# Kernel tuning notes

Measured on AMD Instinct MI355X. Metric: run time of the kernel, lower is better.

The kernel has to match this reference:

```python
import jax, jax.numpy as jnp
import numpy as np

HIDDEN, KEY_DIM, VALUE_DIM = 1024, 64, 64
B, T = 4, 4096


def setup_inputs() -> dict:
    key = jax.random.key(0)
    ks = jax.random.split(key, 9)
    s = 0.02
    return {
        "y_all": jax.random.normal(ks[0], (B, T, HIDDEN), dtype=jnp.float32),
        # torch nn.Linear weights: (out_features, in_features)
        "Wq": jax.random.normal(ks[1], (KEY_DIM, HIDDEN), dtype=jnp.float32) * s,
        "bq": jax.random.normal(ks[2], (KEY_DIM,), dtype=jnp.float32) * s,
        "Wk": jax.random.normal(ks[3], (KEY_DIM, HIDDEN), dtype=jnp.float32) * s,
        "bk": jax.random.normal(ks[4], (KEY_DIM,), dtype=jnp.float32) * s,
        "Wv": jax.random.normal(ks[5], (VALUE_DIM, HIDDEN), dtype=jnp.float32) * s,
        "bv": jax.random.normal(ks[6], (VALUE_DIM,), dtype=jnp.float32) * s,
        "Wo": jax.random.normal(ks[7], (HIDDEN, VALUE_DIM), dtype=jnp.float32) * s,
        "bo": jax.random.normal(ks[8], (HIDDEN,), dtype=jnp.float32) * s,
    }


def reference(y_all, Wq, bq, Wk, bk, Wv, bv, Wo, bo):
    # The original per-timestep loop is exactly causal self-attention:
    # query at position i attends over positions 0..i.
    q = jnp.einsum("bth,kh->btk", y_all, Wq) + bq          # (B,T,Dk)
    k = jnp.einsum("bth,kh->btk", y_all, Wk) + bk          # (B,T,Dk)
    v = jnp.einsum("bth,vh->btv", y_all, Wv) + bv          # (B,T,Dv)
    scale = jnp.asarray(KEY_DIM, q.dtype) ** 0.5
    scores = jnp.einsum("bqk,btk->bqt", q / scale, k)      # (B,T,T)
    t = scores.shape[-1]
    causal = jnp.tril(jnp.ones((t, t), dtype=bool))
    scores = jnp.where(causal, scores, jnp.asarray(-jnp.inf, scores.dtype))
    weights = jax.nn.softmax(scores, axis=-1)
    ctx = jnp.einsum("bqt,btv->bqv", weights, v)           # (B,T,Dv)
    out = jnp.einsum("bqv,hv->bqh", ctx, Wo) + bo          # (B,T,H)
    return out
```

## Files before the change

kernel.cpp:

```cpp
#include <hip/hip_runtime.h>


typedef __attribute__((ext_vector_type(4)))  float f32x4;
typedef __attribute__((ext_vector_type(16))) float f32x16;
typedef __attribute__((ext_vector_type(8)))  short s16x8;
typedef __attribute__((ext_vector_type(4)))  short s16x4;

#define DEV static __device__ __forceinline__

static constexpr int TT = 4096;
static constexpr int HH = 1024;
static constexpr int DD = 64;
static constexpr float MNEG = -3.0e38f;

DEV unsigned short f2bf(float f) {
  union { float f; unsigned int u; } v; v.f = f;
  unsigned int r = v.u + 0x7FFFu + ((v.u >> 16) & 1u);
  return (unsigned short)(r >> 16);
}

DEV unsigned int pk2(float lo, float hi) {
  return (unsigned int)f2bf(lo) | ((unsigned int)f2bf(hi) << 16);
}

DEV s16x8 mk8(unsigned int w0, unsigned int w1, unsigned int w2, unsigned int w3) {
  union { unsigned int u[4]; s16x8 v; } c;
  c.u[0] = w0; c.u[1] = w1; c.u[2] = w2; c.u[3] = w3; return c.v;
}

DEV int swzA(int row) { return ((row & 7) << 4); }
DEV int swzK(int row) { return ((row & 7) << 4) ^ ((row & 8) << 3); }

__global__ void prep_kernel(const float* __restrict__ Wq, const float* __restrict__ Wk,
                            const float* __restrict__ Wv, const float* __restrict__ Wo,
                            unsigned short* __restrict__ Wall,
                            unsigned short* __restrict__ Wo_b)
{
  int i = blockIdx.x * blockDim.x + threadIdx.x;
  int stride = gridDim.x * blockDim.x;
  const int n1 = 64 * HH;
  for (int idx = i; idx < 3 * n1; idx += stride) {
    float v = idx < n1 ? Wq[idx] : (idx < 2 * n1 ? Wk[idx - n1] : Wv[idx - 2 * n1]);
    Wall[idx] = f2bf(v);
  }
  for (int idx = i; idx < HH * DD; idx += stride) {
    int hcol = idx >> 6, d = idx & 63;
    size_t off = (size_t)(hcol >> 4) * 1024 + (d >> 5) * 512 + (hcol & 15) * 32
               + ((d >> 3) & 3) * 8 + (d & 7);
    Wo_b[off] = f2bf(Wo[idx]);
  }
}

__global__ __launch_bounds__(256) void qkv_kernel(
    const float* __restrict__ y, const unsigned short* __restrict__ Wall,
    const float* __restrict__ bq, const float* __restrict__ bk,
    const float* __restrict__ bv,
    unsigned short* __restrict__ q_ws, unsigned short* __restrict__ k_ws,
    unsigned short* __restrict__ vT_ws)
{
  __shared__ unsigned short ylds[2][64 * 64];
  __shared__ unsigned short wlds[2][192 * 64];
  const int t = threadIdx.x;
  const int w = t >> 6, lane = t & 63, g = lane >> 4, c = lane & 15;
  const int row0 = blockIdx.x * 64;
  const int yrow = t >> 2, ycol0 = (t & 3) * 16;

  f32x4 acc[12];
#pragma unroll
  for (int i = 0; i < 12; ++i)
#pragma unroll
    for (int e = 0; e < 4; ++e) acc[i][e] = 0.0f;

  f32x4 yr[4];
  s16x8 wr[6];

  auto load_tiles = [&](int kb) {
    const float* src = y + (size_t)(row0 + yrow) * HH + kb * 64 + ycol0;
    yr[0] = *(const f32x4*)(src);
    yr[1] = *(const f32x4*)(src + 4);
    yr[2] = *(const f32x4*)(src + 8);
    yr[3] = *(const f32x4*)(src + 12);
#pragma unroll
    for (int ii = 0; ii < 6; ++ii) {
      int ch = t + ii * 256;
      int rw = ch >> 3, c0 = (ch & 7) * 8;
      wr[ii] = *(const s16x8*)(Wall + (size_t)rw * HH + kb * 64 + c0);
    }
  };
  auto write_tiles = [&](int buf) {
    s16x8 h0, h1;
#pragma unroll
    for (int e = 0; e < 4; ++e) {
      h0[e]     = (short)f2bf(yr[0][e]);
      h0[e + 4] = (short)f2bf(yr[1][e]);
      h1[e]     = (short)f2bf(yr[2][e]);
      h1[e + 4] = (short)f2bf(yr[3][e]);
    }
    int byte0 = yrow * 128 + ycol0 * 2;
    *(s16x8*)((char*)ylds[buf] + (byte0 ^ swzA(yrow)))        = h0;
    *(s16x8*)((char*)ylds[buf] + ((byte0 + 16) ^ swzA(yrow))) = h1;
#pragma unroll
    for (int ii = 0; ii < 6; ++ii) {
      int ch = t + ii * 256;
      int rw = ch >> 3, c0 = (ch & 7) * 8;
      int byte = rw * 128 + c0 * 2;
      *(s16x8*)((char*)wlds[buf] + (byte ^ swzA(rw))) = wr[ii];
    }
  };

  load_tiles(0);
  write_tiles(0);
  __syncthreads();
  for (int kb = 0; kb < 16; ++kb) {
    int buf = kb & 1;
    if (kb < 15) load_tiles(kb + 1);
#pragma unroll
    for (int kk = 0; kk < 2; ++kk) {
      int r = 16 * w + c;
      s16x8 a = *(const s16x8*)((char*)ylds[buf] +
                  ((r * 128 + (kk * 32 + 8 * g) * 2) ^ swzA(r)));
#pragma unroll
      for (int nt = 0; nt < 12; ++nt) {
        int rb = 16 * nt + c;
        s16x8 b = *(const s16x8*)((char*)wlds[buf] +
                    ((rb * 128 + (kk * 32 + 8 * g) * 2) ^ swzA(rb)));
        acc[nt] = __builtin_amdgcn_mfma_f32_16x16x32_bf16(a, b, acc[nt], 0, 0, 0);
      }
    }
    __syncthreads();
    if (kb < 15) { write_tiles((kb + 1) & 1); __syncthreads(); }
  }

  const float qsc = 1.4426950408889634f / 8.0f;
  const int bb = row0 >> 12;
  const int tb = row0 & 4095;
#pragma unroll
  for (int nt = 0; nt < 12; ++nt) {
    int sec = nt >> 2;
    int dcol = (nt & 3) * 16 + c;
    float bias = sec == 0 ? bq[dcol] : (sec == 1 ? bk[dcol] : bv[dcol]);
    if (sec == 2) {
      s16x4 pv;
#pragma unroll
      for (int i = 0; i < 4; ++i) pv[i] = (short)f2bf(acc[nt][i] + bias);
      int t0 = tb + 16 * w + 4 * g;
      size_t off = (size_t)bb * (DD * TT) + (size_t)(t0 >> 6) * 4096
                 + (dcol >> 5) * 2048 + w * 512 + (dcol & 31) * 16 + (t0 & 15);
      *(s16x4*)(vT_ws + off) = pv;
    } else {
      unsigned short* dst = sec == 0 ? q_ws : k_ws;
      int kk = nt & 3;
#pragma unroll
      for (int i = 0; i < 4; ++i) {
        int t_in = tb + 16 * w + 4 * g + i;
        float val = acc[nt][i] + bias;
        if (sec == 0) val *= qsc;
        size_t off = (size_t)bb * (TT * DD) + (size_t)(t_in >> 5) * 2048
                   + kk * 512 + (t_in & 31) * 16 + c;
        dst[off] = f2bf(val);
      }
    }
  }
}

__global__ __launch_bounds__(256, 2) void attn_kernel(
    const unsigned short* __restrict__ q_ws, const unsigned short* __restrict__ k_ws,
    const unsigned short* __restrict__ vT_ws, const unsigned short* __restrict__ Wo_b,
    const float* __restrict__ bo, float* __restrict__ out)
{
  __shared__ float obuf[3 * 2048];
  __shared__ float mstat[3 * 128];
  __shared__ unsigned short clds[32 * 64];
  const int t = threadIdx.x, wv = t >> 6, lane = t & 63;
  const int qcol = lane & 31, h = lane >> 5;
  const int b = blockIdx.x & 3;
  const int jslot = blockIdx.x >> 2;
  const int j32 = (jslot < 64) ? (2 * jslot) : (127 - 2 * (jslot - 64));
  const int q0 = j32 * 32;
  const int L = j32 >> 1;
  const size_t base  = (size_t)b * TT * DD;
  const size_t vbase = (size_t)b * DD * TT;
  const int g = lane >> 4, c = lane & 15;
  const int lchunk = (lane & 31) * 16 + (lane >> 5) * 8;

  s16x8 qf[4];
  {
    const unsigned short* qp = q_ws + base + (size_t)j32 * 2048;
#pragma unroll
    for (int kk = 0; kk < 4; ++kk) qf[kk] = *(const s16x8*)(qp + kk * 512 + lchunk);
  }
  f32x16 o[2];
#pragma unroll
  for (int mt = 0; mt < 2; ++mt)
#pragma unroll
    for (int rg = 0; rg < 16; ++rg) o[mt][rg] = 0.0f;
  float m_run = MNEG, l_run = 0.0f;

  for (int kt = wv; kt <= L; kt += 4) {
    const int kv0 = kt * 64;
    s16x8 kf[2][4];
#pragma unroll
    for (int mt = 0; mt < 2; ++mt)
#pragma unroll
      for (int kk = 0; kk < 4; ++kk)
        kf[mt][kk] = *(const s16x8*)(k_ws + base +
                       (size_t)(2 * kt + mt) * 2048 + kk * 512 + lchunk);
    f32x16 s[2];
#pragma unroll
    for (int mt = 0; mt < 2; ++mt)
#pragma unroll
      for (int rg = 0; rg < 16; ++rg) s[mt][rg] = 0.0f;
    __builtin_amdgcn_s_setprio(1);
#pragma unroll
    for (int kk = 0; kk < 4; ++kk)
#pragma unroll
      for (int mt = 0; mt < 2; ++mt)
        s[mt] = __builtin_amdgcn_mfma_f32_32x32x16_bf16(kf[mt][kk], qf[kk], s[mt], 0, 0, 0);
    __builtin_amdgcn_s_setprio(0);
    s16x8 vf[2][4];
#pragma unroll
    for (int mt = 0; mt < 2; ++mt)
#pragma unroll
      for (int ks = 0; ks < 4; ++ks)
        vf[mt][ks] = *(const s16x8*)(vT_ws + vbase +
                       (size_t)kt * 4096 + mt * 2048 + ks * 512 + lchunk);
    if (kt == L) {
      int qq = q0 + qcol;
#pragma unroll
      for (int mt = 0; mt < 2; ++mt)
#pragma unroll
        for (int rg = 0; rg < 16; ++rg) {
          int kvabs = kv0 + 32 * mt + (rg & 3) + 8 * (rg >> 2) + 4 * h;
          if (kvabs > qq) s[mt][rg] = MNEG;
        }
    }
    float mx[16];
#pragma unroll
    for (int e = 0; e < 16; ++e) mx[e] = fmaxf(s[0][e], s[1][e]);
#pragma unroll
    for (int st = 8; st >= 1; st >>= 1)
#pragma unroll
      for (int e = 0; e < 8; ++e) if (e < st) mx[e] = fmaxf(mx[e], mx[e + st]);
    float pm = fmaxf(mx[0], __shfl_xor(mx[0], 32));
    float m_new = fmaxf(m_run, pm);
    float alpha = exp2f(m_run - m_new);
#pragma unroll
    for (int mt = 0; mt < 2; ++mt)
#pragma unroll
      for (int rg = 0; rg < 16; ++rg) s[mt][rg] = exp2f(s[mt][rg] - m_new);
    float sm[16];
#pragma unroll
    for (int e = 0; e < 16; ++e) sm[e] = s[0][e] + s[1][e];
#pragma unroll
    for (int st = 8; st >= 1; st >>= 1)
#pragma unroll
      for (int e = 0; e < 8; ++e) if (e < st) sm[e] += sm[e + st];
    float rowsum = sm[0] + __shfl_xor(sm[0], 32);
    l_run = l_run * alpha + rowsum;
    m_run = m_new;
#pragma unroll
    for (int mt = 0; mt < 2; ++mt)
#pragma unroll
      for (int rg = 0; rg < 16; ++rg) o[mt][rg] *= alpha;
    s16x8 pf[4];
#pragma unroll
    for (int mt = 0; mt < 2; ++mt) {
      unsigned int a0 = pk2(s[mt][0],  s[mt][1]);
      unsigned int a1 = pk2(s[mt][2],  s[mt][3]);
      unsigned int b0 = pk2(s[mt][4],  s[mt][5]);
      unsigned int b1 = pk2(s[mt][6],  s[mt][7]);
      unsigned int c0 = pk2(s[mt][8],  s[mt][9]);
      unsigned int c1 = pk2(s[mt][10], s[mt][11]);
      unsigned int d0 = pk2(s[mt][12], s[mt][13]);
      unsigned int d1 = pk2(s[mt][14], s[mt][15]);
      unsigned int t0 = __shfl_xor(h ? a0 : b0, 32);
      unsigned int t1 = __shfl_xor(h ? a1 : b1, 32);
      unsigned int t2 = __shfl_xor(h ? c0 : d0, 32);
      unsigned int t3 = __shfl_xor(h ? c1 : d1, 32);
      pf[2 * mt]     = mk8(h ? t0 : a0, h ? t1 : a1, h ? b0 : t0, h ? b1 : t1);
      pf[2 * mt + 1] = mk8(h ? t2 : c0, h ? t3 : c1, h ? d0 : t2, h ? d1 : t3);
    }
    __builtin_amdgcn_s_setprio(1);
#pragma unroll
    for (int ks = 0; ks < 4; ++ks)
#pragma unroll
      for (int mt = 0; mt < 2; ++mt)
        o[mt] = __builtin_amdgcn_mfma_f32_32x32x16_bf16(vf[mt][ks], pf[ks], o[mt], 0, 0, 0);
    __builtin_amdgcn_s_setprio(0);
  }

  if (wv != 0) {
#pragma unroll
    for (int mt = 0; mt < 2; ++mt)
#pragma unroll
      for (int rg = 0; rg < 16; ++rg)
        obuf[(wv - 1) * 2048 + (mt * 16 + rg) * 64 + lane] = o[mt][rg];
    mstat[(wv - 1) * 128 + lane] = m_run;
    mstat[(wv - 1) * 128 + 64 + lane] = l_run;
  }
  __syncthreads();
  if (wv == 0) {
    float mB[3], lB[3];
    float mS = m_run;
#pragma unroll
    for (int i = 0; i < 3; ++i) {
      mB[i] = mstat[i * 128 + lane];
      lB[i] = mstat[i * 128 + 64 + lane];
      mS = fmaxf(mS, mB[i]);
    }
    float f0 = exp2f(m_run - mS);
    float fi[3];
    float l_tot = l_run * f0;
#pragma unroll
    for (int i = 0; i < 3; ++i) { fi[i] = exp2f(mB[i] - mS); l_tot += lB[i] * fi[i]; }
    float inv = 1.0f / l_tot;
#pragma unroll
    for (int mt = 0; mt < 2; ++mt) {
#pragma unroll
      for (int rgq = 0; rgq < 4; ++rgq) {
        s16x4 pb;
#pragma unroll
        for (int e = 0; e < 4; ++e) {
          int rg = 4 * rgq + e;
          float val = o[mt][rg] * f0;
#pragma unroll
          for (int i = 0; i < 3; ++i)
            val += obuf[i * 2048 + (mt * 16 + rg) * 64 + lane] * fi[i];
          pb[e] = (short)f2bf(val * inv);
        }
        int d0 = 32 * mt + 8 * rgq + 4 * h;
        int byte = qcol * 128 + d0 * 2;
        *(s16x4*)((char*)clds + (byte ^ swzK(qcol))) = pb;
      }
    }
  }
  __syncthreads();

  s16x8 afr[2][2];
#pragma unroll
  for (int mt = 0; mt < 2; ++mt)
#pragma unroll
    for (int kk = 0; kk < 2; ++kk) {
      int ra = 16 * mt + c;
      afr[mt][kk] = *(const s16x8*)((char*)clds +
                      ((ra * 128 + (32 * kk + 8 * g) * 2) ^ swzK(ra)));
    }
  const int wchunk = (lane & 15) * 32 + (lane >> 4) * 8;
  const size_t orow0 = (size_t)(b * TT + q0);
#pragma unroll 4
  for (int nt = 0; nt < 16; ++nt) {
    int col = wv * 256 + 16 * nt + c;
    s16x8 bfr[2];
#pragma unroll
    for (int kk = 0; kk < 2; ++kk)
      bfr[kk] = *(const s16x8*)(Wo_b + (size_t)(wv * 16 + nt) * 1024
                                + kk * 512 + wchunk);
    f32x4 acc4[2];
#pragma unroll
    for (int mt = 0; mt < 2; ++mt)
#pragma unroll
      for (int e = 0; e < 4; ++e) acc4[mt][e] = 0.0f;
#pragma unroll
    for (int kk = 0; kk < 2; ++kk)
#pragma unroll
      for (int mt = 0; mt < 2; ++mt)
        acc4[mt] = __builtin_amdgcn_mfma_f32_16x16x32_bf16(afr[mt][kk], bfr[kk],
                                                           acc4[mt], 0, 0, 0);
    float bias = bo[col];
#pragma unroll
    for (int mt = 0; mt < 2; ++mt)
#pragma unroll
      for (int i = 0; i < 4; ++i) {
        size_t row = orow0 + 16 * mt + 4 * g + i;
        out[row * HH + col] = acc4[mt][i] + bias;
      }
  }
}

extern "C" void kernel_launch(void* const* d_in, const int* in_sizes, int n_in,
                              void* d_out, int out_size, void* d_ws, size_t ws_size,
                              hipStream_t stream)
{
  const float* y  = (const float*)d_in[0];
  const float* Wq = (const float*)d_in[1];
  const float* bq = (const float*)d_in[2];
  const float* Wk = (const float*)d_in[3];
  const float* bk = (const float*)d_in[4];
  const float* Wv = (const float*)d_in[5];
  const float* bv = (const float*)d_in[6];
  const float* Wo = (const float*)d_in[7];
  const float* bo = (const float*)d_in[8];
  float* out = (float*)d_out;
  char* ws = (char*)d_ws;
  unsigned short* Wall  = (unsigned short*)(ws);
  unsigned short* Wo_b  = (unsigned short*)(ws + 393216);
  unsigned short* q_ws  = (unsigned short*)(ws + 524288);
  unsigned short* k_ws  = (unsigned short*)(ws + 524288 + 2097152);
  unsigned short* vT_ws = (unsigned short*)(ws + 524288 + 2 * 2097152);

  prep_kernel<<<dim3(256), dim3(256), 0, stream>>>(Wq, Wk, Wv, Wo, Wall, Wo_b);
  qkv_kernel<<<dim3(256), dim3(256), 0, stream>>>(y, Wall, bq, bk, bv, q_ws, k_ws, vT_ws);
  attn_kernel<<<dim3(512), dim3(256), 0, stream>>>(q_ws, k_ws, vT_ws, Wo_b, bo, out);
}
```

Before: 64.75 us.

## Pack complementary causal query tiles into one 512-thread block for load balance

Each block now has 512 threads split into two 256-thread halves. One half handles query tile u and the other handles tile 127-u, so every block does roughly the same amount of causal work. Shared buffers are doubled per half and the grid is halved to 256 blocks. The aim is to remove the tail imbalance left by the earlier per-block interleaved ordering. The costs are that block-wide syncs now couple two halves with unequal loop lengths, shared memory and register pressure per block grow, and occupancy may drop.

```diff
diff --git a/kernel.cpp b/kernel.cpp
--- a/kernel.cpp
+++ b/kernel.cpp
@@ -163,19 +163,20 @@
   }
 }
 
-__global__ __launch_bounds__(256, 2) void attn_kernel(
+__global__ __launch_bounds__(512, 2) void attn_kernel(
     const unsigned short* __restrict__ q_ws, const unsigned short* __restrict__ k_ws,
     const unsigned short* __restrict__ vT_ws, const unsigned short* __restrict__ Wo_b,
     const float* __restrict__ bo, float* __restrict__ out)
 {
-  __shared__ float obuf[3 * 2048];
-  __shared__ float mstat[3 * 128];
-  __shared__ unsigned short clds[32 * 64];
+  __shared__ float obuf[2][3 * 2048];
+  __shared__ float mstat[2][3 * 128];
+  __shared__ unsigned short clds[2][32 * 64];
   const int t = threadIdx.x, wv = t >> 6, lane = t & 63;
+  const int sub = wv >> 2, wv4 = wv & 3;
   const int qcol = lane & 31, h = lane >> 5;
   const int b = blockIdx.x & 3;
-  const int jslot = blockIdx.x >> 2;
-  const int j32 = (jslot < 64) ? (2 * jslot) : (127 - 2 * (jslot - 64));
+  const int u = blockIdx.x >> 2;
+  const int j32 = sub ? (127 - u) : u;
   const int q0 = j32 * 32;
   const int L = j32 >> 1;
   const size_t base  = (size_t)b * TT * DD;
@@ -196,7 +197,7 @@
     for (int rg = 0; rg < 16; ++rg) o[mt][rg] = 0.0f;
   float m_run = MNEG, l_run = 0.0f;
 
-  for (int kt = wv; kt <= L; kt += 4) {
+  for (int kt = wv4; kt <= L; kt += 4) {
     const int kv0 = kt * 64;
     s16x8 kf[2][4];
 #pragma unroll
@@ -289,23 +290,24 @@
     __builtin_amdgcn_s_setprio(0);
   }
 
-  if (wv != 0) {
+  if (wv4 != 0) {
+    float* ob = &obuf[sub][(wv4 - 1) * 2048];
 #pragma unroll
     for (int mt = 0; mt < 2; ++mt)
 #pragma unroll
       for (int rg = 0; rg < 16; ++rg)
-        obuf[(wv - 1) * 2048 + (mt * 16 + rg) * 64 + lane] = o[mt][rg];
-    mstat[(wv - 1) * 128 + lane] = m_run;
-    mstat[(wv - 1) * 128 + 64 + lane] = l_run;
+        ob[(mt * 16 + rg) * 64 + lane] = o[mt][rg];
+    mstat[sub][(wv4 - 1) * 128 + lane] = m_run;
+    mstat[sub][(wv4 - 1) * 128 + 64 + lane] = l_run;
   }
   __syncthreads();
-  if (wv == 0) {
+  if (wv4 == 0) {
     float mB[3], lB[3];
     float mS = m_run;
 #pragma unroll
     for (int i = 0; i < 3; ++i) {
-      mB[i] = mstat[i * 128 + lane];
-      lB[i] = mstat[i * 128 + 64 + lane];
+      mB[i] = mstat[sub][i * 128 + lane];
+      lB[i] = mstat[sub][i * 128 + 64 + lane];
       mS = fmaxf(mS, mB[i]);
     }
     float f0 = exp2f(m_run - mS);
@@ -325,12 +327,12 @@
           float val = o[mt][rg] * f0;
 #pragma unroll
           for (int i = 0; i < 3; ++i)
-            val += obuf[i * 2048 + (mt * 16 + rg) * 64 + lane] * fi[i];
+            val += obuf[sub][i * 2048 + (mt * 16 + rg) * 64 + lane] * fi[i];
           pb[e] = (short)f2bf(val * inv);
         }
         int d0 = 32 * mt + 8 * rgq + 4 * h;
         int byte = qcol * 128 + d0 * 2;
-        *(s16x4*)((char*)clds + (byte ^ swzK(qcol))) = pb;
+        *(s16x4*)((char*)clds[sub] + (byte ^ swzK(qcol))) = pb;
       }
     }
   }
@@ -342,18 +344,18 @@
 #pragma unroll
     for (int kk = 0; kk < 2; ++kk) {
       int ra = 16 * mt + c;
-      afr[mt][kk] = *(const s16x8*)((char*)clds +
+      afr[mt][kk] = *(const s16x8*)((char*)clds[sub] +
                       ((ra * 128 + (32 * kk + 8 * g) * 2) ^ swzK(ra)));
     }
   const int wchunk = (lane & 15) * 32 + (lane >> 4) * 8;
   const size_t orow0 = (size_t)(b * TT + q0);
 #pragma unroll 4
   for (int nt = 0; nt < 16; ++nt) {
-    int col = wv * 256 + 16 * nt + c;
+    int col = wv4 * 256 + 16 * nt + c;
     s16x8 bfr[2];
 #pragma unroll
     for (int kk = 0; kk < 2; ++kk)
-      bfr[kk] = *(const s16x8*)(Wo_b + (size_t)(wv * 16 + nt) * 1024
+      bfr[kk] = *(const s16x8*)(Wo_b + (size_t)(wv4 * 16 + nt) * 1024
                                 + kk * 512 + wchunk);
     f32x4 acc4[2];
 #pragma unroll
@@ -400,5 +402,5 @@
 
   prep_kernel<<<dim3(256), dim3(256), 0, stream>>>(Wq, Wk, Wv, Wo, Wall, Wo_b);
   qkv_kernel<<<dim3(256), dim3(256), 0, stream>>>(y, Wall, bq, bk, bv, q_ws, k_ws, vT_ws);
-  attn_kernel<<<dim3(512), dim3(256), 0, stream>>>(q_ws, k_ws, vT_ws, Wo_b, bo, out);
-}
+  attn_kernel<<<dim3(256), dim3(512), 0, stream>>>(q_ws, k_ws, vT_ws, Wo_b, bo, out);
+}
```

Result: slower. 68.24 us (+5.4%).
